# Optimization experiments

Hardware: AMD Instinct MI355X
Metric: run time of the kernel (lower is better)

The kernel has to match this reference:

```python
import jax, jax.numpy as jnp
import numpy as np

EPS = 1e-8
LAM = 0.7  # resonance_lambda


def phase_resonance(a, b, eps=EPS):
    # a, b: (B, N, D) float32. Pairwise phase coherence -> (B, N, N)
    D = a.shape[-1]
    pairs = (D // 2)
    a2 = a[..., :pairs * 2].reshape(*a.shape[:-1], pairs, 2)
    b2 = b[..., :pairs * 2].reshape(*b.shape[:-1], pairs, 2)
    theta_a = jnp.arctan2(a2[..., 1] + eps, a2[..., 0] + eps)  # (B,N,pairs)
    theta_b = jnp.arctan2(b2[..., 1] + eps, b2[..., 0] + eps)  # (B,N,pairs)
    delta = theta_a[:, :, None, :] - theta_b[:, None, :, :]    # (B,N,N,pairs)
    return jnp.cos(delta).mean(axis=-1)                        # (B,N,N)


def setup_inputs() -> dict:
    key = jax.random.key(0)
    k1, k2, k3, k4, k5 = jax.random.split(key, 5)
    B, N, D = 2, 1024, 128
    node_states = jax.random.normal(k1, (B, N, D), dtype=jnp.float32)
    node_gates = jax.random.uniform(k2, (B, N, 1), dtype=jnp.float32)
    r_acc = jax.random.normal(k3, (B, N, N), dtype=jnp.float32)
    # nn.Linear(D, D, bias=False) weights, y = x @ W.T
    scale = 1.0 / np.sqrt(D)
    W_in = jax.random.uniform(k4, (D, D), dtype=jnp.float32, minval=-scale, maxval=scale)
    W_out = jax.random.uniform(k5, (D, D), dtype=jnp.float32, minval=-scale, maxval=scale)
    conductance = jnp.asarray(1.0, dtype=jnp.float32)
    return {"node_states": node_states, "node_gates": node_gates, "r_acc": r_acc,
            "W_in": W_in, "W_out": W_out, "conductance": conductance}


def reference(node_states, node_gates, r_acc, W_in, W_out, conductance):
    B, N, D = node_states.shape
    h = node_states @ W_in.T                                   # field_in projection
    r_instant = phase_resonance(h, h)                          # (B,N,N)
    r_acc_new = LAM * r_acc + (1.0 - LAM) * r_instant
    r_acc_new = jnp.clip(r_acc_new, -2.0, 2.0)
    cond = jnp.clip(conductance, -5.0, 5.0)
    coupling = jax.nn.sigmoid(cond * r_acc_new)                # (B,N,N)
    eye = jnp.eye(N, dtype=coupling.dtype)[None]               # zero self-coupling
    coupling = coupling * (1.0 - eye)
    coupling = coupling * jnp.swapaxes(node_gates, -1, -2)     # (B,1,N) col gates
    coupling = coupling * node_gates                           # (B,N,1) row gates
    coupling = coupling / (coupling.sum(axis=-1, keepdims=True) + 1e-8)
    transmitted = node_states * node_gates
    values = transmitted @ W_out.T                             # field_out projection
    field_signal = coupling @ values                           # (B,N,D)
    return field_signal, r_acc_new
```

## Files before the change

### kernel.cpp

```cpp
#include <hip/hip_runtime.h>
#include <hip/hip_bf16.h>

using bf16x8 = __attribute__((ext_vector_type(8))) short;
using f32x4  = __attribute__((ext_vector_type(4))) float;

#define NN 1024
#define DD 128

__device__ __forceinline__ short bf16b(float f) {
    __hip_bfloat16 t = __float2bfloat16(f);
    return *(short*)&t;
}

__device__ __forceinline__ bf16x8 cvt8(const float* __restrict__ p) {
    float4 a = *(const float4*)p;
    float4 b = *(const float4*)(p + 4);
    bf16x8 r;
    r[0] = bf16b(a.x); r[1] = bf16b(a.y); r[2] = bf16b(a.z); r[3] = bf16b(a.w);
    r[4] = bf16b(b.x); r[5] = bf16b(b.y); r[6] = bf16b(b.z); r[7] = bf16b(b.w);
    return r;
}

__global__ __launch_bounds__(256) void prep_kernel(
    const float* __restrict__ states, const float* __restrict__ gates,
    const float* __restrict__ W_in, const float* __restrict__ W_out,
    __hip_bfloat16* __restrict__ M_bf, __hip_bfloat16* __restrict__ valT)
{
    __shared__ __align__(16) short s_m[16][136];
    __shared__ __align__(16) short s_vT[128][24];

    const int tid = threadIdx.x;
    const int l = tid & 63, w = tid >> 6;
    const int row_a = l & 15, kg = l >> 4;
    const int b  = blockIdx.x >> 6;
    const int n0 = (blockIdx.x & 63) * 16;
    const int colbase = w * 32;

    const float* A = states + ((size_t)b * NN + n0) * DD;

    f32x4 accH[2], accV[2];
    #pragma unroll
    for (int cp = 0; cp < 2; ++cp) {
        accH[cp] = (f32x4){0.f, 0.f, 0.f, 0.f};
        accV[cp] = (f32x4){0.f, 0.f, 0.f, 0.f};
    }

    #pragma unroll
    for (int ks = 0; ks < 4; ++ks) {
        int koff = (ks * 4 + kg) * 8;
        bf16x8 a = cvt8(A + row_a * DD + koff);
        #pragma unroll
        for (int cp = 0; cp < 2; ++cp) {
            int d = colbase + cp * 16 + row_a;
            bf16x8 b1 = cvt8(W_in  + d * DD + koff);
            bf16x8 b2 = cvt8(W_out + d * DD + koff);
            accH[cp] = __builtin_amdgcn_mfma_f32_16x16x32_bf16(a, b1, accH[cp], 0, 0, 0);
            accV[cp] = __builtin_amdgcn_mfma_f32_16x16x32_bf16(a, b2, accV[cp], 0, 0, 0);
        }
    }

    float g[4];
    #pragma unroll
    for (int q = 0; q < 4; ++q) g[q] = gates[b * NN + n0 + kg * 4 + q];

    const bool odd = (row_a & 1) != 0;
    #pragma unroll
    for (int cp = 0; cp < 2; ++cp) {
        #pragma unroll
        for (int q = 0; q < 4; ++q) {
            float hm = accH[cp][q] + 1e-8f;
            float hp = __shfl_xor(hm, 1);
            float x = odd ? hp : hm;
            float y = odd ? hm : hp;
            float r2 = x * x + y * y;
            float out;
            if (r2 > 0.f) out = (odd ? y : x) * rsqrtf(r2);
            else          out = odd ? 0.f : 1.f;
            s_m[kg * 4 + q][colbase + cp * 16 + row_a] = bf16b(out);
            s_vT[colbase + cp * 16 + row_a][kg * 4 + q] = bf16b(accV[cp][q] * g[q]);
        }
    }
    __syncthreads();

    {
        int r = tid >> 4, seg = tid & 15;
        bf16x8 v = *(const bf16x8*)&s_m[r][seg * 8];
        *(bf16x8*)(M_bf + ((size_t)b * NN + n0 + r) * DD + seg * 8) = v;
    }
    {
        int d = tid >> 1, half = tid & 1;
        bf16x8 v = *(const bf16x8*)&s_vT[d][half * 8];
        *(bf16x8*)(valT + ((size_t)b * DD + d) * NN + n0 + half * 8) = v;
    }
}

__global__ __launch_bounds__(256) void fused_kernel(
    const __hip_bfloat16* __restrict__ M_bf,
    const __hip_bfloat16* __restrict__ valT,
    const float* __restrict__ r_acc,
    const float* __restrict__ gates,
    const float* __restrict__ cond_ptr,
    float* __restrict__ r_out,
    float* __restrict__ field)
{
    __shared__ __align__(16) short s_cpl[16][136];
    __shared__ float s_rs[16][4];
    __shared__ float s_gate[NN];

    const int tid = threadIdx.x;
    const int l = tid & 63, w = tid >> 6;
    const int row_a = l & 15, kg = l >> 4;
    const int b  = blockIdx.x >> 6;
    const int i0 = (blockIdx.x & 63) * 16;

    const bf16x8* Mv = (const bf16x8*)(M_bf + (size_t)b * NN * DD);
    const bf16x8* Vv = (const bf16x8*)(valT + (size_t)b * DD * NN);

    ((float4*)s_gate)[tid] = ((const float4*)(gates + (size_t)b * NN))[tid];

    bf16x8 aF[4];
    #pragma unroll
    for (int ks = 0; ks < 4; ++ks)
        aF[ks] = Mv[(size_t)(i0 + row_a) * 16 + ks * 4 + kg];

    const float cond = fminf(fmaxf(cond_ptr[0], -5.f), 5.f);
    float g_i[4];
    #pragma unroll
    for (int q = 0; q < 4; ++q) g_i[q] = gates[(size_t)b * NN + i0 + kg * 4 + q];

    const size_t robase = (size_t)b * NN * NN;
    float rs[4] = {0.f, 0.f, 0.f, 0.f};
    f32x4 pacc[2];
    pacc[0] = (f32x4){0.f, 0.f, 0.f, 0.f};
    pacc[1] = (f32x4){0.f, 0.f, 0.f, 0.f};

    __syncthreads();

    for (int jc = 0; jc < 8; ++jc) {
        const int j0 = jc * 128;

        f32x4 acc[2];
        acc[0] = (f32x4){0.f, 0.f, 0.f, 0.f};
        acc[1] = (f32x4){0.f, 0.f, 0.f, 0.f};
        #pragma unroll
        for (int ks = 0; ks < 4; ++ks) {
            #pragma unroll
            for (int cp = 0; cp < 2; ++cp) {
                bf16x8 bb = Mv[(size_t)(j0 + w * 32 + cp * 16 + row_a) * 16 + ks * 4 + kg];
                acc[cp] = __builtin_amdgcn_mfma_f32_16x16x32_bf16(aF[ks], bb, acc[cp], 0, 0, 0);
            }
        }

        #pragma unroll
        for (int q = 0; q < 4; ++q) {
            const int i = i0 + kg * 4 + q;
            const float gi = g_i[q];
            #pragma unroll
            for (int cp = 0; cp < 2; ++cp) {
                const int jl = w * 32 + cp * 16 + row_a;
                const int j  = j0 + jl;
                float s  = acc[cp][q] * (1.f / 64.f);
                float ra = r_acc[robase + (size_t)i * NN + j];
                float rn = fminf(fmaxf(0.7f * ra + 0.3f * s, -2.f), 2.f);
                r_out[robase + (size_t)i * NN + j] = rn;
                float cpl = (i == j) ? 0.f
                            : (1.f / (1.f + __expf(-cond * rn))) * gi * s_gate[j];
                rs[q] += cpl;
                s_cpl[kg * 4 + q][jl] = bf16b(cpl);
            }
        }
        __syncthreads();

        #pragma unroll
        for (int ks2 = 0; ks2 < 4; ++ks2) {
            bf16x8 a = *(const bf16x8*)&s_cpl[row_a][(ks2 * 4 + kg) * 8];
            #pragma unroll
            for (int dt = 0; dt < 2; ++dt) {
                int d = w * 32 + dt * 16 + row_a;
                bf16x8 bb = Vv[(size_t)d * (NN / 8) + jc * 16 + ks2 * 4 + kg];
                pacc[dt] = __builtin_amdgcn_mfma_f32_16x16x32_bf16(a, bb, pacc[dt], 0, 0, 0);
            }
        }
        __syncthreads();
    }

    #pragma unroll
    for (int q = 0; q < 4; ++q) {
        float v = rs[q];
        v += __shfl_xor(v, 1);
        v += __shfl_xor(v, 2);
        v += __shfl_xor(v, 4);
        v += __shfl_xor(v, 8);
        if (row_a == 0) s_rs[kg * 4 + q][w] = v;
    }
    __syncthreads();

    #pragma unroll
    for (int q = 0; q < 4; ++q) {
        const int i = i0 + kg * 4 + q;
        float rsum = s_rs[kg * 4 + q][0] + s_rs[kg * 4 + q][1]
                   + s_rs[kg * 4 + q][2] + s_rs[kg * 4 + q][3];
        float inv = 1.0f / (rsum + 1e-8f);
        #pragma unroll
        for (int dt = 0; dt < 2; ++dt) {
            int d = w * 32 + dt * 16 + row_a;
            field[((size_t)b * NN + i) * DD + d] = pacc[dt][q] * inv;
        }
    }
}

extern "C" void kernel_launch(void* const* d_in, const int* in_sizes, int n_in,
                              void* d_out, int out_size, void* d_ws, size_t ws_size,
                              hipStream_t stream) {
    const float* states = (const float*)d_in[0];
    const float* gates  = (const float*)d_in[1];
    const float* r_acc  = (const float*)d_in[2];
    const float* W_in   = (const float*)d_in[3];
    const float* W_out  = (const float*)d_in[4];
    const float* cond   = (const float*)d_in[5];

    float* field = (float*)d_out;
    float* r_out = field + 2 * NN * DD;

    char* ws = (char*)d_ws;
    __hip_bfloat16* M_bf = (__hip_bfloat16*)ws;
    __hip_bfloat16* valT = (__hip_bfloat16*)(ws + (512 << 10));

    hipLaunchKernelGGL(prep_kernel, dim3(128), dim3(256), 0, stream,
                       states, gates, W_in, W_out, M_bf, valT);
    hipLaunchKernelGGL(fused_kernel, dim3(128), dim3(256), 0, stream,
                       M_bf, valT, r_acc, gates, cond, r_out, field);
}
```

Before: 119.0 us.

## Split the fused kernel over column chunks and reduce partials in a separate kernel

The fused kernel's grid becomes (8,64,2), so each block handles a single 128-column chunk instead of looping over all eight. This raises the block count from 128 to 1024 so that more compute units are filled. Each block writes bf16 partial field sums and row sums to workspace, and a new reduce kernel adds the eight partials and normalises. The trade-offs are an extra launch, extra global traffic for the partials, and rounding the partials to bf16 before they are summed.

```diff
diff --git a/kernel.cpp b/kernel.cpp
--- a/kernel.cpp
+++ b/kernel.cpp
@@ -101,87 +101,63 @@
     const float* __restrict__ gates,
     const float* __restrict__ cond_ptr,
     float* __restrict__ r_out,
-    float* __restrict__ field)
+    __hip_bfloat16* __restrict__ part,
+    float* __restrict__ part_rs)
 {
     __shared__ __align__(16) short s_cpl[16][136];
     __shared__ float s_rs[16][4];
-    __shared__ float s_gate[NN];
 
     const int tid = threadIdx.x;
     const int l = tid & 63, w = tid >> 6;
     const int row_a = l & 15, kg = l >> 4;
-    const int b  = blockIdx.x >> 6;
-    const int i0 = (blockIdx.x & 63) * 16;
+    const int jq = blockIdx.x;
+    const int j0 = jq * 128;
+    const int i0 = blockIdx.y * 16;
+    const int b  = blockIdx.z;
 
     const bf16x8* Mv = (const bf16x8*)(M_bf + (size_t)b * NN * DD);
     const bf16x8* Vv = (const bf16x8*)(valT + (size_t)b * DD * NN);
 
-    ((float4*)s_gate)[tid] = ((const float4*)(gates + (size_t)b * NN))[tid];
-
-    bf16x8 aF[4];
-    #pragma unroll
-    for (int ks = 0; ks < 4; ++ks)
-        aF[ks] = Mv[(size_t)(i0 + row_a) * 16 + ks * 4 + kg];
+    f32x4 acc[2];
+    acc[0] = (f32x4){0.f, 0.f, 0.f, 0.f};
+    acc[1] = (f32x4){0.f, 0.f, 0.f, 0.f};
+    #pragma unroll
+    for (int ks = 0; ks < 4; ++ks) {
+        bf16x8 a = Mv[(size_t)(i0 + row_a) * 16 + ks * 4 + kg];
+        #pragma unroll
+        for (int cp = 0; cp < 2; ++cp) {
+            bf16x8 bb = Mv[(size_t)(j0 + w * 32 + cp * 16 + row_a) * 16 + ks * 4 + kg];
+            acc[cp] = __builtin_amdgcn_mfma_f32_16x16x32_bf16(a, bb, acc[cp], 0, 0, 0);
+        }
+    }
 
     const float cond = fminf(fmaxf(cond_ptr[0], -5.f), 5.f);
-    float g_i[4];
+    float g_i[4], g_j[2];
     #pragma unroll
     for (int q = 0; q < 4; ++q) g_i[q] = gates[(size_t)b * NN + i0 + kg * 4 + q];
+    #pragma unroll
+    for (int cp = 0; cp < 2; ++cp) g_j[cp] = gates[(size_t)b * NN + j0 + w * 32 + cp * 16 + row_a];
 
     const size_t robase = (size_t)b * NN * NN;
     float rs[4] = {0.f, 0.f, 0.f, 0.f};
-    f32x4 pacc[2];
-    pacc[0] = (f32x4){0.f, 0.f, 0.f, 0.f};
-    pacc[1] = (f32x4){0.f, 0.f, 0.f, 0.f};
-
-    __syncthreads();
-
-    for (int jc = 0; jc < 8; ++jc) {
-        const int j0 = jc * 128;
-
-        f32x4 acc[2];
-        acc[0] = (f32x4){0.f, 0.f, 0.f, 0.f};
-        acc[1] = (f32x4){0.f, 0.f, 0.f, 0.f};
-        #pragma unroll
-        for (int ks = 0; ks < 4; ++ks) {
-            #pragma unroll
-            for (int cp = 0; cp < 2; ++cp) {
-                bf16x8 bb = Mv[(size_t)(j0 + w * 32 + cp * 16 + row_a) * 16 + ks * 4 + kg];
-                acc[cp] = __builtin_amdgcn_mfma_f32_16x16x32_bf16(aF[ks], bb, acc[cp], 0, 0, 0);
-            }
-        }
-
-        #pragma unroll
-        for (int q = 0; q < 4; ++q) {
-            const int i = i0 + kg * 4 + q;
-            const float gi = g_i[q];
-            #pragma unroll
-            for (int cp = 0; cp < 2; ++cp) {
-                const int jl = w * 32 + cp * 16 + row_a;
-                const int j  = j0 + jl;
-                float s  = acc[cp][q] * (1.f / 64.f);
-                float ra = r_acc[robase + (size_t)i * NN + j];
-                float rn = fminf(fmaxf(0.7f * ra + 0.3f * s, -2.f), 2.f);
-                r_out[robase + (size_t)i * NN + j] = rn;
-                float cpl = (i == j) ? 0.f
-                            : (1.f / (1.f + __expf(-cond * rn))) * gi * s_gate[j];
-                rs[q] += cpl;
-                s_cpl[kg * 4 + q][jl] = bf16b(cpl);
-            }
-        }
-        __syncthreads();
-
-        #pragma unroll
-        for (int ks2 = 0; ks2 < 4; ++ks2) {
-            bf16x8 a = *(const bf16x8*)&s_cpl[row_a][(ks2 * 4 + kg) * 8];
-            #pragma unroll
-            for (int dt = 0; dt < 2; ++dt) {
-                int d = w * 32 + dt * 16 + row_a;
-                bf16x8 bb = Vv[(size_t)d * (NN / 8) + jc * 16 + ks2 * 4 + kg];
-                pacc[dt] = __builtin_amdgcn_mfma_f32_16x16x32_bf16(a, bb, pacc[dt], 0, 0, 0);
-            }
-        }
-        __syncthreads();
+
+    #pragma unroll
+    for (int q = 0; q < 4; ++q) {
+        const int i = i0 + kg * 4 + q;
+        const float gi = g_i[q];
+        #pragma unroll
+        for (int cp = 0; cp < 2; ++cp) {
+            const int jl = w * 32 + cp * 16 + row_a;
+            const int j  = j0 + jl;
+            float s  = acc[cp][q] * (1.f / 64.f);
+            float ra = r_acc[robase + (size_t)i * NN + j];
+            float rn = fminf(fmaxf(0.7f * ra + 0.3f * s, -2.f), 2.f);
+            r_out[robase + (size_t)i * NN + j] = rn;
+            float cpl = (i == j) ? 0.f
+                        : (1.f / (1.f + __expf(-cond * rn))) * gi * g_j[cp];
+            rs[q] += cpl;
+            s_cpl[kg * 4 + q][jl] = bf16b(cpl);
+        }
     }
 
     #pragma unroll
@@ -195,18 +171,62 @@
     }
     __syncthreads();
 
-    #pragma unroll
-    for (int q = 0; q < 4; ++q) {
-        const int i = i0 + kg * 4 + q;
-        float rsum = s_rs[kg * 4 + q][0] + s_rs[kg * 4 + q][1]
-                   + s_rs[kg * 4 + q][2] + s_rs[kg * 4 + q][3];
-        float inv = 1.0f / (rsum + 1e-8f);
+    f32x4 pacc[2];
+    pacc[0] = (f32x4){0.f, 0.f, 0.f, 0.f};
+    pacc[1] = (f32x4){0.f, 0.f, 0.f, 0.f};
+    #pragma unroll
+    for (int ks2 = 0; ks2 < 4; ++ks2) {
+        bf16x8 a = *(const bf16x8*)&s_cpl[row_a][(ks2 * 4 + kg) * 8];
         #pragma unroll
         for (int dt = 0; dt < 2; ++dt) {
             int d = w * 32 + dt * 16 + row_a;
-            field[((size_t)b * NN + i) * DD + d] = pacc[dt][q] * inv;
-        }
-    }
+            bf16x8 bb = Vv[(size_t)d * (NN / 8) + (j0 >> 3) + ks2 * 4 + kg];
+            pacc[dt] = __builtin_amdgcn_mfma_f32_16x16x32_bf16(a, bb, pacc[dt], 0, 0, 0);
+        }
+    }
+
+    __hip_bfloat16* pb = part + ((size_t)jq * 2 + b) * NN * DD;
+    #pragma unroll
+    for (int dt = 0; dt < 2; ++dt) {
+        #pragma unroll
+        for (int q = 0; q < 4; ++q) {
+            int i = i0 + kg * 4 + q;
+            int d = w * 32 + dt * 16 + row_a;
+            pb[(size_t)i * DD + d] = __float2bfloat16(pacc[dt][q]);
+        }
+    }
+
+    if (tid < 16)
+        part_rs[((size_t)jq * 2 + b) * NN + i0 + tid] =
+            s_rs[tid][0] + s_rs[tid][1] + s_rs[tid][2] + s_rs[tid][3];
+}
+
+__global__ __launch_bounds__(256) void reduce_kernel(
+    const __hip_bfloat16* __restrict__ part,
+    const float* __restrict__ part_rs,
+    float* __restrict__ field)
+{
+    int t   = blockIdx.x * 256 + threadIdx.x;
+    int b   = t >> 15;
+    int rem = t & 32767;
+    int i   = rem >> 5;
+    int d4  = (rem & 31) * 4;
+    size_t ibase = (size_t)i * DD + d4;
+
+    float s0 = 0.f, s1 = 0.f, s2 = 0.f, s3 = 0.f, rsum = 0.f;
+    #pragma unroll
+    for (int jq = 0; jq < 8; ++jq) {
+        size_t slab = ((size_t)jq * 2 + b);
+        uint2 u = *(const uint2*)(part + slab * NN * DD + ibase);
+        s0 += __uint_as_float(u.x << 16);
+        s1 += __uint_as_float(u.x & 0xffff0000u);
+        s2 += __uint_as_float(u.y << 16);
+        s3 += __uint_as_float(u.y & 0xffff0000u);
+        rsum += part_rs[slab * NN + i];
+    }
+    float inv = 1.0f / (rsum + 1e-8f);
+    float4 o = {s0 * inv, s1 * inv, s2 * inv, s3 * inv};
+    *(float4*)(field + ((size_t)b * NN + i) * DD + d4) = o;
 }
 
 extern "C" void kernel_launch(void* const* d_in, const int* in_sizes, int n_in,
@@ -223,11 +243,15 @@
     float* r_out = field + 2 * NN * DD;
 
     char* ws = (char*)d_ws;
-    __hip_bfloat16* M_bf = (__hip_bfloat16*)ws;
-    __hip_bfloat16* valT = (__hip_bfloat16*)(ws + (512 << 10));
+    __hip_bfloat16* M_bf    = (__hip_bfloat16*)ws;
+    __hip_bfloat16* valT    = (__hip_bfloat16*)(ws + (512 << 10));
+    __hip_bfloat16* part    = (__hip_bfloat16*)(ws + (1 << 20));
+    float*          part_rs = (float*)(ws + (5 << 20));
 
     hipLaunchKernelGGL(prep_kernel, dim3(128), dim3(256), 0, stream,
                        states, gates, W_in, W_out, M_bf, valT);
-    hipLaunchKernelGGL(fused_kernel, dim3(128), dim3(256), 0, stream,
-                       M_bf, valT, r_acc, gates, cond, r_out, field);
-}
+    hipLaunchKernelGGL(fused_kernel, dim3(8, 64, 2), dim3(256), 0, stream,
+                       M_bf, valT, r_acc, gates, cond, r_out, part, part_rs);
+    hipLaunchKernelGGL(reduce_kernel, dim3(256), dim3(256), 0, stream,
+                       part, part_rs, field);
+}
```

Result: faster. 97.73 us (-17.9%).
